# Kernel tuning notes

Hardware: AMD Instinct MI355X
Metric: run time of the kernel (lower is better)

Reference implementation:

```python
import jax, jax.numpy as jnp
import numpy as np

B = 256          # graph pairs
S = 128          # max_set_size (all graphs full-size)
D = 64           # node_state_dim (= filters_3)
DE = 32          # encoded edge dim
DM = 128         # message dim
DT = 32          # transform_dim
IN_N, IN_E = 16, 8
EPG = 1024       # edges per graph
NPROP = 5
SINK_ITERS = 20
TEMP = 0.1
N = 2 * B * S    # total nodes
E = 2 * B * EPG  # total edges


def setup_inputs() -> dict:
    key = jax.random.key(0)
    ks = jax.random.split(key, 32)
    def w(k, shp):
        return (jax.random.normal(k, shp, jnp.float32) / np.sqrt(shp[0])).astype(jnp.float32)
    base = jnp.repeat(jnp.arange(2 * B, dtype=jnp.int64) * S, EPG)
    from_idx = base + jax.random.randint(ks[0], (E,), 0, S).astype(jnp.int64)
    to_idx = base + jax.random.randint(ks[1], (E,), 0, S).astype(jnp.int64)
    return {
        'node_features': jax.random.normal(ks[2], (N, IN_N), jnp.float32),
        'edge_features': jax.random.normal(ks[3], (E, IN_E), jnp.float32),
        'W_enc_n': w(ks[4], (IN_N, D)),  'b_enc_n': jnp.zeros((D,), jnp.float32),
        'W_enc_e': w(ks[5], (IN_E, DE)), 'b_enc_e': jnp.zeros((DE,), jnp.float32),
        'W_c1': w(ks[6], (2 * D, 2 * D)), 'b_c1': jnp.zeros((2 * D,), jnp.float32),
        'W_c2': w(ks[7], (2 * D, D)),     'b_c2': jnp.zeros((D,), jnp.float32),
        'W_m1': w(ks[8], (2 * D + DE, DM)), 'b_m1': jnp.zeros((DM,), jnp.float32),
        'W_m2': w(ks[9], (DM, DM)),         'b_m2': jnp.zeros((DM,), jnp.float32),
        'W_u1': w(ks[10], (D + DM, DM)), 'b_u1': jnp.zeros((DM,), jnp.float32),
        'W_u2': w(ks[11], (DM, D)),      'b_u2': jnp.zeros((D,), jnp.float32),
        'W_t1': w(ks[12], (D, DT)), 'b_t1': jnp.zeros((DT,), jnp.float32),
        'W_t2': w(ks[13], (DT, DT)), 'b_t2': jnp.zeros((DT,), jnp.float32),
        'from_idx': from_idx, 'to_idx': to_idx,
    }


def _sinkhorn(sim):
    # log-space sinkhorn normalization, fixed iteration count
    log_a = sim / TEMP
    for _ in range(SINK_ITERS):
        log_a = log_a - jax.nn.logsumexp(log_a, axis=2, keepdims=True)
        log_a = log_a - jax.nn.logsumexp(log_a, axis=1, keepdims=True)
    return jnp.exp(log_a)


def reference(node_features, edge_features, W_enc_n, b_enc_n, W_enc_e, b_enc_e,
              W_c1, b_c1, W_c2, b_c2, W_m1, b_m1, W_m2, b_m2,
              W_u1, b_u1, W_u2, b_u2, W_t1, b_t1, W_t2, b_t2,
              from_idx, to_idx):
    h_enc = node_features @ W_enc_n + b_enc_n          # [N, D]
    e_enc = edge_features @ W_enc_e + b_enc_e          # [E, DE]

    def prop(h):
        # bidirectional messages, shared params (GMN GraphPropLayer, mlp update)
        hf, ht = h[from_idx], h[to_idx]
        m_f = jnp.concatenate([hf, ht, e_enc], -1)
        m_f = jax.nn.relu(m_f @ W_m1 + b_m1) @ W_m2 + b_m2
        m_r = jnp.concatenate([ht, hf, e_enc], -1)
        m_r = jax.nn.relu(m_r @ W_m1 + b_m1) @ W_m2 + b_m2
        agg = jax.ops.segment_sum(m_f, to_idx, num_segments=N) \
            + jax.ops.segment_sum(m_r, from_idx, num_segments=N)
        u = jnp.concatenate([h, agg], -1)
        return jax.nn.relu(u @ W_u1 + b_u1) @ W_u2 + b_u2

    h = h_enc
    store = jnp.zeros_like(h_enc)
    for _ in range(NPROP):
        comb = jnp.concatenate([h, store], -1)
        comb = jax.nn.relu(comb @ W_c1 + b_c1) @ W_c2 + b_c2
        h = prop(comb)                                  # [N, D]
        padded = h.reshape(2 * B, S, D)                 # full graphs -> pad is reshape
        q, c = padded[0::2], padded[1::2]               # [B, S, D] each
        tq = jax.nn.relu(q @ W_t1 + b_t1) @ W_t2 + b_t2
        tc = jax.nn.relu(c @ W_t1 + b_t1) @ W_t2 + b_t2
        # masks are all-ones since every graph has S nodes
        sim = jnp.einsum('bid,bjd->bij', tq, tc)        # [B, S, S]
        T = _sinkhorn(sim)
        q_from_c = jnp.einsum('bij,bjd->bid', T, c)
        c_from_q = jnp.einsum('bij,bid->bjd', T, q)
        # interleave q0,c0,q1,c1,... then gather by node_indices (= arange here)
        store = jnp.stack([q_from_c, c_from_q], axis=1).reshape(N, D)
    scores = -jnp.sum(jax.nn.relu(q - jnp.einsum('bij,bjd->bid', T, c)), axis=(1, 2))
    return scores
```

## Files before the change

kernel.cpp:

```cpp
#include <hip/hip_runtime.h>
#include <hip/hip_bf16.h>

#define NNODE  65536
#define NEDGE  524288
#define NGRAPH 512
#define EPG    1024
#define NPROP  5
#define SINKI  20

typedef __attribute__((ext_vector_type(4))) float f32x4;
typedef __attribute__((ext_vector_type(8))) _Float16 f16x8;

template<int IN, int OUT>
__global__ void enc_kernel(const float* __restrict__ x, const float* __restrict__ W,
                           const float* __restrict__ b, float* __restrict__ y, int rows) {
    int idx = blockIdx.x * blockDim.x + threadIdx.x;
    if (idx >= rows * OUT) return;
    int r = idx / OUT, o = idx % OUT;
    const float* xr = x + (size_t)r * IN;
    float acc = b[o];
#pragma unroll
    for (int k = 0; k < IN; ++k) acc = fmaf(xr[k], W[k * OUT + o], acc);
    y[idx] = acc;
}

template<int IN1, int IN2, int HID, int OUT>
__global__ __launch_bounds__(256) void mlp2_kernel(
    const float* __restrict__ x1, const float* __restrict__ x2,
    const float* __restrict__ W1, const float* __restrict__ b1,
    const float* __restrict__ W2, const float* __restrict__ b2,
    float* __restrict__ y) {
    constexpr int IN = IN1 + IN2;
    constexpr int TR = 64;
    __shared__ float xs[TR][IN];
    __shared__ float hs[TR][HID];
    const int t = threadIdx.x;
    const int row0 = blockIdx.x * TR;

    constexpr int INQ = IN / 4;
    for (int idx = t; idx < TR * INQ; idx += 256) {
        int r = idx / INQ, k0 = (idx % INQ) * 4;
        float4 v;
        if (IN2 == 0 || k0 < IN1) v = *(const float4*)(x1 + (size_t)(row0 + r) * IN1 + k0);
        else                      v = *(const float4*)(x2 + (size_t)(row0 + r) * IN2 + (k0 - IN1));
        *(float4*)&xs[r][k0] = v;
    }
    __syncthreads();

    constexpr int HQ = HID / 4;
    for (int idx = t; idx < TR * HQ; idx += 256) {
        int r = idx / HQ, j0 = (idx % HQ) * 4;
        float a0 = b1[j0], a1 = b1[j0+1], a2 = b1[j0+2], a3 = b1[j0+3];
        const float* wp = W1 + j0;
#pragma unroll 8
        for (int k = 0; k < IN; ++k) {
            float xv = xs[r][k];
            float4 w = *(const float4*)(wp + k * HID);
            a0 = fmaf(xv, w.x, a0); a1 = fmaf(xv, w.y, a1);
            a2 = fmaf(xv, w.z, a2); a3 = fmaf(xv, w.w, a3);
        }
        hs[r][j0]   = fmaxf(a0, 0.f); hs[r][j0+1] = fmaxf(a1, 0.f);
        hs[r][j0+2] = fmaxf(a2, 0.f); hs[r][j0+3] = fmaxf(a3, 0.f);
    }
    __syncthreads();

    constexpr int OQ = OUT / 4;
    for (int idx = t; idx < TR * OQ; idx += 256) {
        int r = idx / OQ, d0 = (idx % OQ) * 4;
        float a0 = b2[d0], a1 = b2[d0+1], a2 = b2[d0+2], a3 = b2[d0+3];
        const float* wp = W2 + d0;
#pragma unroll 8
        for (int k = 0; k < HID; ++k) {
            float hv = hs[r][k];
            float4 w = *(const float4*)(wp + k * OUT);
            a0 = fmaf(hv, w.x, a0); a1 = fmaf(hv, w.y, a1);
            a2 = fmaf(hv, w.z, a2); a3 = fmaf(hv, w.w, a3);
        }
        *(float4*)(y + (size_t)(row0 + r) * OUT + d0) = make_float4(a0, a1, a2, a3);
    }
}

union __align__(16) MsgSMem {
    struct {
        float ag[128][128];
        _Float16 csh[128 * 64];
        _Float16 csl[128 * 64];
        _Float16 Hh[64 * 128];
        _Float16 Hl[64 * 128];
        int ef[1024];
        int et[1024];
    } run;
    _Float16 w1p[2][128 * 160];
    _Float16 w2p[2][128 * 128];
};

__global__ __launch_bounds__(512, 2) void msg_kernel(
    const float* __restrict__ c, const float* __restrict__ e_enc,
    const int* __restrict__ from_idx, const int* __restrict__ to_idx,
    const float* __restrict__ W1, const float* __restrict__ b1,
    const float* __restrict__ W2, const float* __restrict__ b2,
    float* __restrict__ agg) {
    __shared__ MsgSMem sm;
    const int g = blockIdx.x, t = threadIdx.x;
    const int l = t & 63, wid = t >> 6;
    const int rg = wid >> 2;
    const int cg = wid & 3;
    const int lr = l & 15;
    const int lk = (l >> 4) * 8;
    const int ebase = g * EPG, nbase = g * 128;

    for (int idx = t; idx < 160 * 128; idx += 512) {
        int k = idx >> 7, cc = idx & 127;
        float v = W1[idx];
        _Float16 h = (_Float16)v;
        sm.w1p[0][cc * 160 + k] = h;
        sm.w1p[1][cc * 160 + k] = (_Float16)(v - (float)h);
    }
    __syncthreads();
    f16x8 b1h[5][2], b1l[5][2];
#pragma unroll
    for (int kf = 0; kf < 5; ++kf)
#pragma unroll
        for (int cf = 0; cf < 2; ++cf) {
            const int col = cg * 32 + cf * 16 + lr;
            b1h[kf][cf] = *(const f16x8*)&sm.w1p[0][col * 160 + kf * 32 + lk];
            b1l[kf][cf] = *(const f16x8*)&sm.w1p[1][col * 160 + kf * 32 + lk];
        }
    const float b1v0 = b1[cg * 32 + lr], b1v1 = b1[cg * 32 + 16 + lr];
    __syncthreads();

    for (int idx = t; idx < 128 * 128; idx += 512) {
        int k = idx >> 7, cc = idx & 127;
        float v = W2[idx];
        _Float16 h = (_Float16)v;
        sm.w2p[0][cc * 128 + k] = h;
        sm.w2p[1][cc * 128 + k] = (_Float16)(v - (float)h);
    }
    __syncthreads();
    f16x8 b2h[4][2], b2l[4][2];
#pragma unroll
    for (int kf = 0; kf < 4; ++kf)
#pragma unroll
        for (int cf = 0; cf < 2; ++cf) {
            const int col = cg * 32 + cf * 16 + lr;
            b2h[kf][cf] = *(const f16x8*)&sm.w2p[0][col * 128 + kf * 32 + lk];
            b2l[kf][cf] = *(const f16x8*)&sm.w2p[1][col * 128 + kf * 32 + lk];
        }
    const float b2v0 = b2[cg * 32 + lr], b2v1 = b2[cg * 32 + 16 + lr];
    __syncthreads();

    for (int idx = t; idx < 4096; idx += 512)
        ((float4*)sm.run.ag)[idx] = make_float4(0.f, 0.f, 0.f, 0.f);
    {
        const float* cblk = c + (size_t)nbase * 64;
        char* cshB = (char*)sm.run.csh;
        char* cslB = (char*)sm.run.csl;
        for (int idx = t; idx < 128 * 64; idx += 512) {
            int row = idx >> 6, cc = idx & 63;
            float v = cblk[idx];
            _Float16 h = (_Float16)v;
            int byte = ((row << 7) | (cc << 1)) ^ ((row & 7) << 4);
            *(_Float16*)(cshB + byte) = h;
            *(_Float16*)(cslB + byte) = (_Float16)(v - (float)h);
        }
    }
    for (int idx = t; idx < 1024; idx += 512) {
        sm.run.ef[idx] = from_idx[ebase + idx] - nbase;
        sm.run.et[idx] = to_idx[ebase + idx] - nbase;
    }
    __syncthreads();

    char* cshB = (char*)sm.run.csh;
    char* cslB = (char*)sm.run.csl;
    char* HhB  = (char*)sm.run.Hh;
    char* HlB  = (char*)sm.run.Hl;

    for (int tile = 0; tile < 32; ++tile) {
        f32x4 acc[2][2];
#pragma unroll
        for (int rf = 0; rf < 2; ++rf) {
            const int rloc = rg * 32 + rf * 16 + lr;
            const int R = tile * 64 + rloc;
            const int el = R >> 1, dir = R & 1;
            const int fi = sm.run.ef[el], ti = sm.run.et[el];
            const int rA = dir ? ti : fi;
            const int rB = dir ? fi : ti;
            const int swA = (rA & 7) << 4, swB = (rB & 7) << 4;
            f16x8 ah[5], al[5];
            ah[0] = *(const f16x8*)(cshB + (((rA << 7) | (lk << 1)) ^ swA));
            al[0] = *(const f16x8*)(cslB + (((rA << 7) | (lk << 1)) ^ swA));
            ah[1] = *(const f16x8*)(cshB + (((rA << 7) | ((32 + lk) << 1)) ^ swA));
            al[1] = *(const f16x8*)(cslB + (((rA << 7) | ((32 + lk) << 1)) ^ swA));
            ah[2] = *(const f16x8*)(cshB + (((rB << 7) | (lk << 1)) ^ swB));
            al[2] = *(const f16x8*)(cslB + (((rB << 7) | (lk << 1)) ^ swB));
            ah[3] = *(const f16x8*)(cshB + (((rB << 7) | ((32 + lk) << 1)) ^ swB));
            al[3] = *(const f16x8*)(cslB + (((rB << 7) | ((32 + lk) << 1)) ^ swB));
            {
                const float* eE = e_enc + (size_t)(ebase + el) * 32 + lk;
                const float4 e0 = *(const float4*)eE;
                const float4 e1 = *(const float4*)(eE + 4);
                float ev[8] = {e0.x, e0.y, e0.z, e0.w, e1.x, e1.y, e1.z, e1.w};
                f16x8 h8, l8;
#pragma unroll
                for (int j = 0; j < 8; ++j) {
                    _Float16 h = (_Float16)ev[j];
                    h8[j] = h;
                    l8[j] = (_Float16)(ev[j] - (float)h);
                }
                ah[4] = h8; al[4] = l8;
            }
            acc[rf][0] = (f32x4){b1v0, b1v0, b1v0, b1v0};
            acc[rf][1] = (f32x4){b1v1, b1v1, b1v1, b1v1};
#pragma unroll
            for (int kf = 0; kf < 5; ++kf)
#pragma unroll
                for (int cf = 0; cf < 2; ++cf) {
                    acc[rf][cf] = __builtin_amdgcn_mfma_f32_16x16x32_f16(ah[kf], b1h[kf][cf], acc[rf][cf], 0, 0, 0);
                    acc[rf][cf] = __builtin_amdgcn_mfma_f32_16x16x32_f16(al[kf], b1h[kf][cf], acc[rf][cf], 0, 0, 0);
                    acc[rf][cf] = __builtin_amdgcn_mfma_f32_16x16x32_f16(ah[kf], b1l[kf][cf], acc[rf][cf], 0, 0, 0);
                }
        }
        __syncthreads();
#pragma unroll
        for (int rf = 0; rf < 2; ++rf)
#pragma unroll
            for (int cf = 0; cf < 2; ++cf) {
                const int col = cg * 32 + cf * 16 + lr;
#pragma unroll
                for (int q = 0; q < 4; ++q) {
                    const int row = rg * 32 + rf * 16 + (l >> 4) * 4 + q;
                    const int byte = ((row << 8) | (col << 1)) ^ ((row & 7) << 4);
                    float v = fmaxf(acc[rf][cf][q], 0.f);
                    _Float16 h = (_Float16)v;
                    *(_Float16*)(HhB + byte) = h;
                    *(_Float16*)(HlB + byte) = (_Float16)(v - (float)h);
                }
            }
        __syncthreads();

#pragma unroll
        for (int rf = 0; rf < 2; ++rf) {
            const int row = rg * 32 + rf * 16 + lr;
            const int sw = (row & 7) << 4;
            f16x8 xh[4], xl[4];
#pragma unroll
            for (int kf = 0; kf < 4; ++kf) {
                const int byte = ((row << 8) | ((kf * 32 + lk) << 1)) ^ sw;
                xh[kf] = *(const f16x8*)(HhB + byte);
                xl[kf] = *(const f16x8*)(HlB + byte);
            }
            f32x4 acc2[2];
            acc2[0] = (f32x4){b2v0, b2v0, b2v0, b2v0};
            acc2[1] = (f32x4){b2v1, b2v1, b2v1, b2v1};
#pragma unroll
            for (int kf = 0; kf < 4; ++kf)
#pragma unroll
                for (int cf = 0; cf < 2; ++cf) {
                    acc2[cf] = __builtin_amdgcn_mfma_f32_16x16x32_f16(xh[kf], b2h[kf][cf], acc2[cf], 0, 0, 0);
                    acc2[cf] = __builtin_amdgcn_mfma_f32_16x16x32_f16(xl[kf], b2h[kf][cf], acc2[cf], 0, 0, 0);
                    acc2[cf] = __builtin_amdgcn_mfma_f32_16x16x32_f16(xh[kf], b2l[kf][cf], acc2[cf], 0, 0, 0);
                }
            const int r0 = rg * 32 + rf * 16 + ((l >> 4) << 2);
            const int e0 = (tile * 64 + r0) >> 1;
            int dst[4];
            dst[0] = sm.run.et[e0];
            dst[1] = sm.run.ef[e0];
            dst[2] = sm.run.et[e0 + 1];
            dst[3] = sm.run.ef[e0 + 1];
#pragma unroll
            for (int q = 0; q < 4; ++q)
#pragma unroll
                for (int cf = 0; cf < 2; ++cf)
                    atomicAdd(&sm.run.ag[dst[q]][cg * 32 + cf * 16 + lr], acc2[cf][q]);
        }
    }
    __syncthreads();
    float* aout = agg + (size_t)g * 128 * 128;
    for (int idx = t; idx < 4096; idx += 512)
        ((float4*)aout)[idx] = ((const float4*)sm.run.ag)[idx];
}

__global__ __launch_bounds__(256) void sink_kernel(
    const float* __restrict__ tbuf, const float* __restrict__ h,
    float* __restrict__ store, float* __restrict__ scores, int do_score) {
    __shared__ float la[128][128];
    __shared__ float ub[2 * 128 * 66];
    __shared__ float pm[256], ps[256];
    const int p = blockIdx.x, t = threadIdx.x;

    const float* tq_src = tbuf + (size_t)(2 * p)     * 128 * 32;
    const float* tc_src = tbuf + (size_t)(2 * p + 1) * 128 * 32;
    for (int idx = t; idx < 4096; idx += 256) {
        int i = idx >> 5, k = idx & 31;
        ub[i * 33 + k]            = tq_src[idx];
        ub[128 * 33 + i * 33 + k] = tc_src[idx];
    }
    __syncthreads();

    for (int idx = t; idx < 16384; idx += 256) {
        int i = idx >> 7, j = idx & 127;
        float acc = 0.f;
#pragma unroll
        for (int k = 0; k < 32; ++k)
            acc = fmaf(ub[i * 33 + k], ub[128 * 33 + j * 33 + k], acc);
        la[i][j] = acc * 10.f;
    }
    __syncthreads();

    const int w = t >> 6, l = t & 63;
    for (int iter = 0; iter < SINKI; ++iter) {
        for (int r = w; r < 128; r += 4) {
            float a0 = la[r][l], a1 = la[r][l + 64];
            float mx = fmaxf(a0, a1);
#pragma unroll
            for (int off = 32; off >= 1; off >>= 1) mx = fmaxf(mx, __shfl_xor(mx, off));
            float s = __expf(a0 - mx) + __expf(a1 - mx);
#pragma unroll
            for (int off = 32; off >= 1; off >>= 1) s += __shfl_xor(s, off);
            float lse = mx + __logf(s);
            la[r][l]      = a0 - lse;
            la[r][l + 64] = a1 - lse;
        }
        __syncthreads();
        const int j = t & 127, hh = t >> 7, i0 = hh * 64;
        float mx = -INFINITY;
        for (int i = i0; i < i0 + 64; ++i) mx = fmaxf(mx, la[i][j]);
        pm[t] = mx;
        __syncthreads();
        const float M = fmaxf(pm[j], pm[128 + j]);
        float s = 0.f;
        for (int i = i0; i < i0 + 64; ++i) s += __expf(la[i][j] - M);
        ps[t] = s;
        __syncthreads();
        const float lse = M + __logf(ps[j] + ps[128 + j]);
        for (int i = i0; i < i0 + 64; ++i) la[i][j] -= lse;
        __syncthreads();
    }

    for (int idx = t; idx < 16384; idx += 256)
        ((float*)la)[idx] = __expf(((float*)la)[idx]);
    const float* hq_src = h + (size_t)(2 * p)     * 128 * 64;
    const float* hc_src = h + (size_t)(2 * p + 1) * 128 * 64;
    for (int idx = t; idx < 8192; idx += 256) {
        int i = idx >> 6, d = idx & 63;
        ub[i * 66 + d]            = hq_src[idx];
        ub[128 * 66 + i * 66 + d] = hc_src[idx];
    }
    __syncthreads();

    float sc = 0.f;
    float* store_q = store + (size_t)(2 * p)     * 128 * 64;
    float* store_c = store + (size_t)(2 * p + 1) * 128 * 64;
    for (int idx = t; idx < 8192; idx += 256) {
        int i = idx >> 6, d = idx & 63;
        float acc = 0.f;
#pragma unroll 8
        for (int j = 0; j < 128; ++j)
            acc = fmaf(la[i][j], ub[128 * 66 + j * 66 + d], acc);
        store_q[idx] = acc;
        if (do_score) sc += fmaxf(ub[i * 66 + d] - acc, 0.f);
    }
    for (int idx = t; idx < 8192; idx += 256) {
        int j = idx >> 6, d = idx & 63;
        float acc = 0.f;
#pragma unroll 8
        for (int i = 0; i < 128; ++i)
            acc = fmaf(la[i][j], ub[i * 66 + d], acc);
        store_c[idx] = acc;
    }
    if (do_score) {
#pragma unroll
        for (int off = 32; off >= 1; off >>= 1) sc += __shfl_xor(sc, off);
        if (l == 0) pm[w] = sc;
        __syncthreads();
        if (t == 0) scores[p] = -(pm[0] + pm[1] + pm[2] + pm[3]);
    }
}

extern "C" void kernel_launch(void* const* d_in, const int* in_sizes, int n_in,
                              void* d_out, int out_size, void* d_ws, size_t ws_size,
                              hipStream_t stream) {
    const float* node_features = (const float*)d_in[0];
    const float* edge_features = (const float*)d_in[1];
    const float* W_enc_n = (const float*)d_in[2];
    const float* b_enc_n = (const float*)d_in[3];
    const float* W_enc_e = (const float*)d_in[4];
    const float* b_enc_e = (const float*)d_in[5];
    const float* W_c1 = (const float*)d_in[6];
    const float* b_c1 = (const float*)d_in[7];
    const float* W_c2 = (const float*)d_in[8];
    const float* b_c2 = (const float*)d_in[9];
    const float* W_m1 = (const float*)d_in[10];
    const float* b_m1 = (const float*)d_in[11];
    const float* W_m2 = (const float*)d_in[12];
    const float* b_m2 = (const float*)d_in[13];
    const float* W_u1 = (const float*)d_in[14];
    const float* b_u1 = (const float*)d_in[15];
    const float* W_u2 = (const float*)d_in[16];
    const float* b_u2 = (const float*)d_in[17];
    const float* W_t1 = (const float*)d_in[18];
    const float* b_t1 = (const float*)d_in[19];
    const float* W_t2 = (const float*)d_in[20];
    const float* b_t2 = (const float*)d_in[21];
    const int* from_idx = (const int*)d_in[22];
    const int* to_idx   = (const int*)d_in[23];
    float* scores = (float*)d_out;

    char* ws = (char*)d_ws;
    size_t off = 0;
    auto alloc = [&](size_t nfloats) { float* pp = (float*)(ws + off); off += nfloats * sizeof(float); return pp; };
    float* h    = alloc((size_t)NNODE * 64);
    float* st   = alloc((size_t)NNODE * 64);
    float* cbuf = alloc((size_t)NNODE * 64);
    float* aggb = alloc((size_t)NNODE * 128);
    float* tb   = alloc((size_t)NNODE * 32);
    float* eenc = alloc((size_t)NEDGE * 32);
    (void)ws_size; (void)in_sizes; (void)n_in; (void)out_size;

    hipMemsetAsync(st, 0, (size_t)NNODE * 64 * sizeof(float), stream);
    enc_kernel<16, 64><<<(NNODE * 64 + 255) / 256, 256, 0, stream>>>(node_features, W_enc_n, b_enc_n, h, NNODE);
    enc_kernel<8, 32><<<(NEDGE * 32 + 255) / 256, 256, 0, stream>>>(edge_features, W_enc_e, b_enc_e, eenc, NEDGE);

    for (int it = 0; it < NPROP; ++it) {
        mlp2_kernel<64, 64, 128, 64><<<NNODE / 64, 256, 0, stream>>>(h, st, W_c1, b_c1, W_c2, b_c2, cbuf);
        msg_kernel<<<NGRAPH, 512, 0, stream>>>(cbuf, eenc, from_idx, to_idx, W_m1, b_m1, W_m2, b_m2, aggb);
        mlp2_kernel<64, 128, 128, 64><<<NNODE / 64, 256, 0, stream>>>(cbuf, aggb, W_u1, b_u1, W_u2, b_u2, h);
        mlp2_kernel<64, 0, 32, 32><<<NNODE / 64, 256, 0, stream>>>(h, nullptr, W_t1, b_t1, W_t2, b_t2, tb);
        sink_kernel<<<256, 256, 0, stream>>>(tb, h, st, scores, it == NPROP - 1 ? 1 : 0);
    }
}
```

Baseline: 9.295 ms.

## Presplit message weights and edge encodings, shrink MLP tiles, widen sinkhorn blocks

The fp16 hi/lo splitting of the message MLP weights and edge encodings moves out of every msg_kernel block into one-time prep kernels. Weights now load straight from global into registers, and the shared-memory union is dropped. Hidden activations are stored packed hi/lo in one array, and the aggregation buffer gets an XOR swizzle against bank conflicts. The MLP row tile halves to 32 to launch more blocks, and sinkhorn uses 512 threads with a 4-way column reduction. Together these add extra launches and more shared-memory pressure per block, which may change occupancy.

Measured after the change: 8.210 ms. 1.13x faster.

```diff
diff --git a/kernel.cpp b/kernel.cpp
--- a/kernel.cpp
+++ b/kernel.cpp
@@ -10,6 +10,32 @@
 
 typedef __attribute__((ext_vector_type(4))) float f32x4;
 typedef __attribute__((ext_vector_type(8))) _Float16 f16x8;
+
+static __device__ __forceinline__ void split2(float v, _Float16& h, _Float16& l) {
+    h = (_Float16)v;
+    l = (_Float16)(v - (float)h);
+}
+
+static __device__ __forceinline__ unsigned packsplit(float v) {
+    _Float16 h = (_Float16)v;
+    _Float16 lo2 = (_Float16)(v - (float)h);
+    union { _Float16 f; unsigned short s; } uh, ul;
+    uh.f = h; ul.f = lo2;
+    return (unsigned)uh.s | ((unsigned)ul.s << 16);
+}
+
+static __device__ __forceinline__ void unpack8(uint4 a, uint4 b, f16x8& h, f16x8& l) {
+    union { unsigned u[4]; f16x8 v; } H, L;
+    H.u[0] = (a.x & 0xffffu) | (a.y << 16);
+    H.u[1] = (a.z & 0xffffu) | (a.w << 16);
+    H.u[2] = (b.x & 0xffffu) | (b.y << 16);
+    H.u[3] = (b.z & 0xffffu) | (b.w << 16);
+    L.u[0] = (a.x >> 16) | (a.y & 0xffff0000u);
+    L.u[1] = (a.z >> 16) | (a.w & 0xffff0000u);
+    L.u[2] = (b.x >> 16) | (b.y & 0xffff0000u);
+    L.u[3] = (b.z >> 16) | (b.w & 0xffff0000u);
+    h = H.v; l = L.v;
+}
 
 template<int IN, int OUT>
 __global__ void enc_kernel(const float* __restrict__ x, const float* __restrict__ W,
@@ -24,6 +50,31 @@
     y[idx] = acc;
 }
 
+template<int IN, int OUT>
+__global__ void enc_split_kernel(const float* __restrict__ x, const float* __restrict__ W,
+                                 const float* __restrict__ b,
+                                 _Float16* __restrict__ yh, _Float16* __restrict__ yl, int rows) {
+    int idx = blockIdx.x * blockDim.x + threadIdx.x;
+    if (idx >= rows * OUT) return;
+    int r = idx / OUT, o = idx % OUT;
+    const float* xr = x + (size_t)r * IN;
+    float acc = b[o];
+#pragma unroll
+    for (int k = 0; k < IN; ++k) acc = fmaf(xr[k], W[k * OUT + o], acc);
+    _Float16 h, l; split2(acc, h, l);
+    yh[idx] = h; yl[idx] = l;
+}
+
+__global__ void splitT_kernel(const float* __restrict__ W, _Float16* __restrict__ Wh,
+                              _Float16* __restrict__ Wl, int K, int C) {
+    int idx = blockIdx.x * blockDim.x + threadIdx.x;
+    if (idx >= K * C) return;
+    int k = idx / C, cc = idx % C;
+    _Float16 h, l; split2(W[idx], h, l);
+    Wh[(size_t)cc * K + k] = h;
+    Wl[(size_t)cc * K + k] = l;
+}
+
 template<int IN1, int IN2, int HID, int OUT>
 __global__ __launch_bounds__(256) void mlp2_kernel(
     const float* __restrict__ x1, const float* __restrict__ x2,
@@ -31,7 +82,7 @@
     const float* __restrict__ W2, const float* __restrict__ b2,
     float* __restrict__ y) {
     constexpr int IN = IN1 + IN2;
-    constexpr int TR = 64;
+    constexpr int TR = 32;
     __shared__ float xs[TR][IN];
     __shared__ float hs[TR][HID];
     const int t = threadIdx.x;
@@ -59,8 +110,8 @@
             a0 = fmaf(xv, w.x, a0); a1 = fmaf(xv, w.y, a1);
             a2 = fmaf(xv, w.z, a2); a3 = fmaf(xv, w.w, a3);
         }
-        hs[r][j0]   = fmaxf(a0, 0.f); hs[r][j0+1] = fmaxf(a1, 0.f);
-        hs[r][j0+2] = fmaxf(a2, 0.f); hs[r][j0+3] = fmaxf(a3, 0.f);
+        *(float4*)&hs[r][j0] = make_float4(fmaxf(a0, 0.f), fmaxf(a1, 0.f),
+                                           fmaxf(a2, 0.f), fmaxf(a3, 0.f));
     }
     __syncthreads();
 
@@ -80,100 +131,64 @@
     }
 }
 
-union __align__(16) MsgSMem {
-    struct {
-        float ag[128][128];
-        _Float16 csh[128 * 64];
-        _Float16 csl[128 * 64];
-        _Float16 Hh[64 * 128];
-        _Float16 Hl[64 * 128];
-        int ef[1024];
-        int et[1024];
-    } run;
-    _Float16 w1p[2][128 * 160];
-    _Float16 w2p[2][128 * 128];
-};
-
 __global__ __launch_bounds__(512, 2) void msg_kernel(
-    const float* __restrict__ c, const float* __restrict__ e_enc,
+    const float* __restrict__ c,
+    const _Float16* __restrict__ eh, const _Float16* __restrict__ el,
     const int* __restrict__ from_idx, const int* __restrict__ to_idx,
-    const float* __restrict__ W1, const float* __restrict__ b1,
-    const float* __restrict__ W2, const float* __restrict__ b2,
+    const _Float16* __restrict__ W1h, const _Float16* __restrict__ W1l, const float* __restrict__ b1,
+    const _Float16* __restrict__ W2h, const _Float16* __restrict__ W2l, const float* __restrict__ b2,
     float* __restrict__ agg) {
-    __shared__ MsgSMem sm;
+    __shared__ float ag[128][128];
+    __shared__ _Float16 csh[128 * 64];
+    __shared__ _Float16 csl[128 * 64];
+    __shared__ unsigned Hp[64 * 128];
+    __shared__ int ef[1024], et[1024];
     const int g = blockIdx.x, t = threadIdx.x;
     const int l = t & 63, wid = t >> 6;
-    const int rg = wid >> 2;
-    const int cg = wid & 3;
-    const int lr = l & 15;
-    const int lk = (l >> 4) * 8;
+    const int rg = wid >> 2, cg = wid & 3;
+    const int lr = l & 15, lk = (l >> 4) * 8;
     const int ebase = g * EPG, nbase = g * 128;
 
-    for (int idx = t; idx < 160 * 128; idx += 512) {
-        int k = idx >> 7, cc = idx & 127;
-        float v = W1[idx];
-        _Float16 h = (_Float16)v;
-        sm.w1p[0][cc * 160 + k] = h;
-        sm.w1p[1][cc * 160 + k] = (_Float16)(v - (float)h);
-    }
-    __syncthreads();
-    f16x8 b1h[5][2], b1l[5][2];
+    f16x8 b1h[5][2], b1l[5][2], b2h[4][2], b2l[4][2];
 #pragma unroll
     for (int kf = 0; kf < 5; ++kf)
 #pragma unroll
         for (int cf = 0; cf < 2; ++cf) {
-            const int col = cg * 32 + cf * 16 + lr;
-            b1h[kf][cf] = *(const f16x8*)&sm.w1p[0][col * 160 + kf * 32 + lk];
-            b1l[kf][cf] = *(const f16x8*)&sm.w1p[1][col * 160 + kf * 32 + lk];
-        }
-    const float b1v0 = b1[cg * 32 + lr], b1v1 = b1[cg * 32 + 16 + lr];
-    __syncthreads();
-
-    for (int idx = t; idx < 128 * 128; idx += 512) {
-        int k = idx >> 7, cc = idx & 127;
-        float v = W2[idx];
-        _Float16 h = (_Float16)v;
-        sm.w2p[0][cc * 128 + k] = h;
-        sm.w2p[1][cc * 128 + k] = (_Float16)(v - (float)h);
-    }
-    __syncthreads();
-    f16x8 b2h[4][2], b2l[4][2];
+            int col = cg * 32 + cf * 16 + lr;
+            b1h[kf][cf] = *(const f16x8*)&W1h[(size_t)col * 160 + kf * 32 + lk];
+            b1l[kf][cf] = *(const f16x8*)&W1l[(size_t)col * 160 + kf * 32 + lk];
+        }
 #pragma unroll
     for (int kf = 0; kf < 4; ++kf)
 #pragma unroll
         for (int cf = 0; cf < 2; ++cf) {
-            const int col = cg * 32 + cf * 16 + lr;
-            b2h[kf][cf] = *(const f16x8*)&sm.w2p[0][col * 128 + kf * 32 + lk];
-            b2l[kf][cf] = *(const f16x8*)&sm.w2p[1][col * 128 + kf * 32 + lk];
-        }
-    const float b2v0 = b2[cg * 32 + lr], b2v1 = b2[cg * 32 + 16 + lr];
-    __syncthreads();
+            int col = cg * 32 + cf * 16 + lr;
+            b2h[kf][cf] = *(const f16x8*)&W2h[(size_t)col * 128 + kf * 32 + lk];
+            b2l[kf][cf] = *(const f16x8*)&W2l[(size_t)col * 128 + kf * 32 + lk];
+        }
+    const float b1v[2] = { b1[cg * 32 + lr], b1[cg * 32 + 16 + lr] };
+    const float b2v[2] = { b2[cg * 32 + lr], b2[cg * 32 + 16 + lr] };
 
     for (int idx = t; idx < 4096; idx += 512)
-        ((float4*)sm.run.ag)[idx] = make_float4(0.f, 0.f, 0.f, 0.f);
+        ((float4*)ag)[idx] = make_float4(0.f, 0.f, 0.f, 0.f);
     {
         const float* cblk = c + (size_t)nbase * 64;
-        char* cshB = (char*)sm.run.csh;
-        char* cslB = (char*)sm.run.csl;
-        for (int idx = t; idx < 128 * 64; idx += 512) {
-            int row = idx >> 6, cc = idx & 63;
-            float v = cblk[idx];
-            _Float16 h = (_Float16)v;
-            int byte = ((row << 7) | (cc << 1)) ^ ((row & 7) << 4);
-            *(_Float16*)(cshB + byte) = h;
-            *(_Float16*)(cslB + byte) = (_Float16)(v - (float)h);
+        char* chB = (char*)csh; char* clB = (char*)csl;
+        for (int idx = t; idx < 8192; idx += 512) {
+            int row = idx >> 6, k = idx & 63;
+            _Float16 h, lo2; split2(cblk[idx], h, lo2);
+            int byte = ((row << 7) | (k << 1)) ^ ((row & 7) << 4);
+            *(_Float16*)(chB + byte) = h;
+            *(_Float16*)(clB + byte) = lo2;
         }
     }
     for (int idx = t; idx < 1024; idx += 512) {
-        sm.run.ef[idx] = from_idx[ebase + idx] - nbase;
-        sm.run.et[idx] = to_idx[ebase + idx] - nbase;
-    }
-    __syncthreads();
-
-    char* cshB = (char*)sm.run.csh;
-    char* cslB = (char*)sm.run.csl;
-    char* HhB  = (char*)sm.run.Hh;
-    char* HlB  = (char*)sm.run.Hl;
+        ef[idx] = from_idx[ebase + idx] - nbase;
+        et[idx] = to_idx[ebase + idx] - nbase;
+    }
+    __syncthreads();
+
+    char* chB = (char*)csh; char* clB = (char*)csl;
 
     for (int tile = 0; tile < 32; ++tile) {
         f32x4 acc[2][2];
@@ -181,36 +196,23 @@
         for (int rf = 0; rf < 2; ++rf) {
             const int rloc = rg * 32 + rf * 16 + lr;
             const int R = tile * 64 + rloc;
-            const int el = R >> 1, dir = R & 1;
-            const int fi = sm.run.ef[el], ti = sm.run.et[el];
-            const int rA = dir ? ti : fi;
-            const int rB = dir ? fi : ti;
+            const int e2 = R >> 1, dir = R & 1;
+            const int fi = ef[e2], ti = et[e2];
+            const int rA = dir ? ti : fi, rB = dir ? fi : ti;
             const int swA = (rA & 7) << 4, swB = (rB & 7) << 4;
             f16x8 ah[5], al[5];
-            ah[0] = *(const f16x8*)(cshB + (((rA << 7) | (lk << 1)) ^ swA));
-            al[0] = *(const f16x8*)(cslB + (((rA << 7) | (lk << 1)) ^ swA));
-            ah[1] = *(const f16x8*)(cshB + (((rA << 7) | ((32 + lk) << 1)) ^ swA));
-            al[1] = *(const f16x8*)(cslB + (((rA << 7) | ((32 + lk) << 1)) ^ swA));
-            ah[2] = *(const f16x8*)(cshB + (((rB << 7) | (lk << 1)) ^ swB));
-            al[2] = *(const f16x8*)(cslB + (((rB << 7) | (lk << 1)) ^ swB));
-            ah[3] = *(const f16x8*)(cshB + (((rB << 7) | ((32 + lk) << 1)) ^ swB));
-            al[3] = *(const f16x8*)(cslB + (((rB << 7) | ((32 + lk) << 1)) ^ swB));
-            {
-                const float* eE = e_enc + (size_t)(ebase + el) * 32 + lk;
-                const float4 e0 = *(const float4*)eE;
-                const float4 e1 = *(const float4*)(eE + 4);
-                float ev[8] = {e0.x, e0.y, e0.z, e0.w, e1.x, e1.y, e1.z, e1.w};
-                f16x8 h8, l8;
-#pragma unroll
-                for (int j = 0; j < 8; ++j) {
-                    _Float16 h = (_Float16)ev[j];
-                    h8[j] = h;
-                    l8[j] = (_Float16)(ev[j] - (float)h);
-                }
-                ah[4] = h8; al[4] = l8;
-            }
-            acc[rf][0] = (f32x4){b1v0, b1v0, b1v0, b1v0};
-            acc[rf][1] = (f32x4){b1v1, b1v1, b1v1, b1v1};
+            ah[0] = *(const f16x8*)(chB + (((rA << 7) | (lk << 1)) ^ swA));
+            al[0] = *(const f16x8*)(clB + (((rA << 7) | (lk << 1)) ^ swA));
+            ah[1] = *(const f16x8*)(chB + (((rA << 7) | ((32 + lk) << 1)) ^ swA));
+            al[1] = *(const f16x8*)(clB + (((rA << 7) | ((32 + lk) << 1)) ^ swA));
+            ah[2] = *(const f16x8*)(chB + (((rB << 7) | (lk << 1)) ^ swB));
+            al[2] = *(const f16x8*)(clB + (((rB << 7) | (lk << 1)) ^ swB));
+            ah[3] = *(const f16x8*)(chB + (((rB << 7) | ((32 + lk) << 1)) ^ swB));
+            al[3] = *(const f16x8*)(clB + (((rB << 7) | ((32 + lk) << 1)) ^ swB));
+            ah[4] = *(const f16x8*)&eh[(size_t)(ebase + e2) * 32 + lk];
+            al[4] = *(const f16x8*)&el[(size_t)(ebase + e2) * 32 + lk];
+            acc[rf][0] = (f32x4){b1v[0], b1v[0], b1v[0], b1v[0]};
+            acc[rf][1] = (f32x4){b1v[1], b1v[1], b1v[1], b1v[1]};
 #pragma unroll
             for (int kf = 0; kf < 5; ++kf)
 #pragma unroll
@@ -229,75 +231,69 @@
 #pragma unroll
                 for (int q = 0; q < 4; ++q) {
                     const int row = rg * 32 + rf * 16 + (l >> 4) * 4 + q;
-                    const int byte = ((row << 8) | (col << 1)) ^ ((row & 7) << 4);
-                    float v = fmaxf(acc[rf][cf][q], 0.f);
-                    _Float16 h = (_Float16)v;
-                    *(_Float16*)(HhB + byte) = h;
-                    *(_Float16*)(HlB + byte) = (_Float16)(v - (float)h);
+                    Hp[(row * 128 + col) ^ ((row & 7) << 2)] = packsplit(fmaxf(acc[rf][cf][q], 0.f));
                 }
             }
         __syncthreads();
-
 #pragma unroll
         for (int rf = 0; rf < 2; ++rf) {
             const int row = rg * 32 + rf * 16 + lr;
-            const int sw = (row & 7) << 4;
-            f16x8 xh[4], xl[4];
+            const int sw = (row & 7) << 2;
+            f32x4 acc2[2];
+            acc2[0] = (f32x4){b2v[0], b2v[0], b2v[0], b2v[0]};
+            acc2[1] = (f32x4){b2v[1], b2v[1], b2v[1], b2v[1]};
 #pragma unroll
             for (int kf = 0; kf < 4; ++kf) {
-                const int byte = ((row << 8) | ((kf * 32 + lk) << 1)) ^ sw;
-                xh[kf] = *(const f16x8*)(HhB + byte);
-                xl[kf] = *(const f16x8*)(HlB + byte);
+                const int c0 = kf * 32 + lk;
+                uint4 pa = *(const uint4*)&Hp[(row * 128 + c0) ^ sw];
+                uint4 pb = *(const uint4*)&Hp[(row * 128 + c0 + 4) ^ sw];
+                f16x8 xh, xl; unpack8(pa, pb, xh, xl);
+#pragma unroll
+                for (int cf = 0; cf < 2; ++cf) {
+                    acc2[cf] = __builtin_amdgcn_mfma_f32_16x16x32_f16(xh, b2h[kf][cf], acc2[cf], 0, 0, 0);
+                    acc2[cf] = __builtin_amdgcn_mfma_f32_16x16x32_f16(xl, b2h[kf][cf], acc2[cf], 0, 0, 0);
+                    acc2[cf] = __builtin_amdgcn_mfma_f32_16x16x32_f16(xh, b2l[kf][cf], acc2[cf], 0, 0, 0);
+                }
             }
-            f32x4 acc2[2];
-            acc2[0] = (f32x4){b2v0, b2v0, b2v0, b2v0};
-            acc2[1] = (f32x4){b2v1, b2v1, b2v1, b2v1};
-#pragma unroll
-            for (int kf = 0; kf < 4; ++kf)
-#pragma unroll
-                for (int cf = 0; cf < 2; ++cf) {
-                    acc2[cf] = __builtin_amdgcn_mfma_f32_16x16x32_f16(xh[kf], b2h[kf][cf], acc2[cf], 0, 0, 0);
-                    acc2[cf] = __builtin_amdgcn_mfma_f32_16x16x32_f16(xl[kf], b2h[kf][cf], acc2[cf], 0, 0, 0);
-                    acc2[cf] = __builtin_amdgcn_mfma_f32_16x16x32_f16(xh[kf], b2l[kf][cf], acc2[cf], 0, 0, 0);
-                }
             const int r0 = rg * 32 + rf * 16 + ((l >> 4) << 2);
             const int e0 = (tile * 64 + r0) >> 1;
-            int dst[4];
-            dst[0] = sm.run.et[e0];
-            dst[1] = sm.run.ef[e0];
-            dst[2] = sm.run.et[e0 + 1];
-            dst[3] = sm.run.ef[e0 + 1];
+            int dst[4] = { et[e0], ef[e0], et[e0 + 1], ef[e0 + 1] };
 #pragma unroll
             for (int q = 0; q < 4; ++q)
 #pragma unroll
-                for (int cf = 0; cf < 2; ++cf)
-                    atomicAdd(&sm.run.ag[dst[q]][cg * 32 + cf * 16 + lr], acc2[cf][q]);
+                for (int cf = 0; cf < 2; ++cf) {
+                    const int colq = cg * 32 + cf * 16 + lr;
+                    atomicAdd(&ag[dst[q]][colq ^ ((dst[q] & 7) << 2)], acc2[cf][q]);
+                }
         }
     }
     __syncthreads();
     float* aout = agg + (size_t)g * 128 * 128;
-    for (int idx = t; idx < 4096; idx += 512)
-        ((float4*)aout)[idx] = ((const float4*)sm.run.ag)[idx];
-}
-
-__global__ __launch_bounds__(256) void sink_kernel(
+    for (int idx = t; idx < 4096; idx += 512) {
+        int row = idx >> 5, c4 = (idx & 31) << 2;
+        ((float4*)aout)[idx] = *(const float4*)&ag[row][c4 ^ ((row & 7) << 2)];
+    }
+}
+
+__global__ __launch_bounds__(512) void sink_kernel(
     const float* __restrict__ tbuf, const float* __restrict__ h,
     float* __restrict__ store, float* __restrict__ scores, int do_score) {
     __shared__ float la[128][128];
     __shared__ float ub[2 * 128 * 66];
-    __shared__ float pm[256], ps[256];
+    __shared__ float pm[512], ps[512];
     const int p = blockIdx.x, t = threadIdx.x;
+    const int w = t >> 6, l = t & 63;
 
     const float* tq_src = tbuf + (size_t)(2 * p)     * 128 * 32;
     const float* tc_src = tbuf + (size_t)(2 * p + 1) * 128 * 32;
-    for (int idx = t; idx < 4096; idx += 256) {
+    for (int idx = t; idx < 4096; idx += 512) {
         int i = idx >> 5, k = idx & 31;
         ub[i * 33 + k]            = tq_src[idx];
         ub[128 * 33 + i * 33 + k] = tc_src[idx];
     }
     __syncthreads();
 
-    for (int idx = t; idx < 16384; idx += 256) {
+    for (int idx = t; idx < 16384; idx += 512) {
         int i = idx >> 7, j = idx & 127;
         float acc = 0.f;
 #pragma unroll
@@ -307,9 +303,8 @@
     }
     __syncthreads();
 
-    const int w = t >> 6, l = t & 63;
     for (int iter = 0; iter < SINKI; ++iter) {
-        for (int r = w; r < 128; r += 4) {
+        for (int r = w; r < 128; r += 8) {
             float a0 = la[r][l], a1 = la[r][l + 64];
             float mx = fmaxf(a0, a1);
 #pragma unroll
@@ -322,26 +317,26 @@
             la[r][l + 64] = a1 - lse;
         }
         __syncthreads();
-        const int j = t & 127, hh = t >> 7, i0 = hh * 64;
+        const int j = t & 127, q4 = t >> 7, i0 = q4 * 32;
         float mx = -INFINITY;
-        for (int i = i0; i < i0 + 64; ++i) mx = fmaxf(mx, la[i][j]);
+        for (int i = i0; i < i0 + 32; ++i) mx = fmaxf(mx, la[i][j]);
         pm[t] = mx;
         __syncthreads();
-        const float M = fmaxf(pm[j], pm[128 + j]);
+        const float M = fmaxf(fmaxf(pm[j], pm[j + 128]), fmaxf(pm[j + 256], pm[j + 384]));
         float s = 0.f;
-        for (int i = i0; i < i0 + 64; ++i) s += __expf(la[i][j] - M);
+        for (int i = i0; i < i0 + 32; ++i) s += __expf(la[i][j] - M);
         ps[t] = s;
         __syncthreads();
-        const float lse = M + __logf(ps[j] + ps[128 + j]);
-        for (int i = i0; i < i0 + 64; ++i) la[i][j] -= lse;
-        __syncthreads();
-    }
-
-    for (int idx = t; idx < 16384; idx += 256)
+        const float lse = M + __logf(ps[j] + ps[j + 128] + ps[j + 256] + ps[j + 384]);
+        for (int i = i0; i < i0 + 32; ++i) la[i][j] -= lse;
+        __syncthreads();
+    }
+
+    for (int idx = t; idx < 16384; idx += 512)
         ((float*)la)[idx] = __expf(((float*)la)[idx]);
     const float* hq_src = h + (size_t)(2 * p)     * 128 * 64;
     const float* hc_src = h + (size_t)(2 * p + 1) * 128 * 64;
-    for (int idx = t; idx < 8192; idx += 256) {
+    for (int idx = t; idx < 8192; idx += 512) {
         int i = idx >> 6, d = idx & 63;
         ub[i * 66 + d]            = hq_src[idx];
         ub[128 * 66 + i * 66 + d] = hc_src[idx];
@@ -351,7 +346,7 @@
     float sc = 0.f;
     float* store_q = store + (size_t)(2 * p)     * 128 * 64;
     float* store_c = store + (size_t)(2 * p + 1) * 128 * 64;
-    for (int idx = t; idx < 8192; idx += 256) {
+    for (int idx = t; idx < 8192; idx += 512) {
         int i = idx >> 6, d = idx & 63;
         float acc = 0.f;
 #pragma unroll 8
@@ -360,7 +355,7 @@
         store_q[idx] = acc;
         if (do_score) sc += fmaxf(ub[i * 66 + d] - acc, 0.f);
     }
-    for (int idx = t; idx < 8192; idx += 256) {
+    for (int idx = t; idx < 8192; idx += 512) {
         int j = idx >> 6, d = idx & 63;
         float acc = 0.f;
 #pragma unroll 8
@@ -373,7 +368,12 @@
         for (int off = 32; off >= 1; off >>= 1) sc += __shfl_xor(sc, off);
         if (l == 0) pm[w] = sc;
         __syncthreads();
-        if (t == 0) scores[p] = -(pm[0] + pm[1] + pm[2] + pm[3]);
+        if (t == 0) {
+            float s8 = 0.f;
+#pragma unroll
+            for (int i = 0; i < 8; ++i) s8 += pm[i];
+            scores[p] = -s8;
+        }
     }
 }
 
@@ -408,24 +408,32 @@
 
     char* ws = (char*)d_ws;
     size_t off = 0;
-    auto alloc = [&](size_t nfloats) { float* pp = (float*)(ws + off); off += nfloats * sizeof(float); return pp; };
-    float* h    = alloc((size_t)NNODE * 64);
-    float* st   = alloc((size_t)NNODE * 64);
-    float* cbuf = alloc((size_t)NNODE * 64);
-    float* aggb = alloc((size_t)NNODE * 128);
-    float* tb   = alloc((size_t)NNODE * 32);
-    float* eenc = alloc((size_t)NEDGE * 32);
+    auto alloc = [&](size_t bytes) { char* p = ws + off; off += (bytes + 255) & ~(size_t)255; return p; };
+    float* h    = (float*)alloc((size_t)NNODE * 64 * 4);
+    float* st   = (float*)alloc((size_t)NNODE * 64 * 4);
+    float* cbuf = (float*)alloc((size_t)NNODE * 64 * 4);
+    float* aggb = (float*)alloc((size_t)NNODE * 128 * 4);
+    float* tb   = (float*)alloc((size_t)NNODE * 32 * 4);
+    _Float16* eench = (_Float16*)alloc((size_t)NEDGE * 32 * 2);
+    _Float16* eencl = (_Float16*)alloc((size_t)NEDGE * 32 * 2);
+    _Float16* Wm1h = (_Float16*)alloc(160 * 128 * 2);
+    _Float16* Wm1l = (_Float16*)alloc(160 * 128 * 2);
+    _Float16* Wm2h = (_Float16*)alloc(128 * 128 * 2);
+    _Float16* Wm2l = (_Float16*)alloc(128 * 128 * 2);
     (void)ws_size; (void)in_sizes; (void)n_in; (void)out_size;
 
     hipMemsetAsync(st, 0, (size_t)NNODE * 64 * sizeof(float), stream);
     enc_kernel<16, 64><<<(NNODE * 64 + 255) / 256, 256, 0, stream>>>(node_features, W_enc_n, b_enc_n, h, NNODE);
-    enc_kernel<8, 32><<<(NEDGE * 32 + 255) / 256, 256, 0, stream>>>(edge_features, W_enc_e, b_enc_e, eenc, NEDGE);
+    enc_split_kernel<8, 32><<<(NEDGE * 32 + 255) / 256, 256, 0, stream>>>(edge_features, W_enc_e, b_enc_e, eench, eencl, NEDGE);
+    splitT_kernel<<<(160 * 128 + 255) / 256, 256, 0, stream>>>(W_m1, Wm1h, Wm1l, 160, 128);
+    splitT_kernel<<<(128 * 128 + 255) / 256, 256, 0, stream>>>(W_m2, Wm2h, Wm2l, 128, 128);
 
     for (int it = 0; it < NPROP; ++it) {
-        mlp2_kernel<64, 64, 128, 64><<<NNODE / 64, 256, 0, stream>>>(h, st, W_c1, b_c1, W_c2, b_c2, cbuf);
-        msg_kernel<<<NGRAPH, 512, 0, stream>>>(cbuf, eenc, from_idx, to_idx, W_m1, b_m1, W_m2, b_m2, aggb);
-        mlp2_kernel<64, 128, 128, 64><<<NNODE / 64, 256, 0, stream>>>(cbuf, aggb, W_u1, b_u1, W_u2, b_u2, h);
-        mlp2_kernel<64, 0, 32, 32><<<NNODE / 64, 256, 0, stream>>>(h, nullptr, W_t1, b_t1, W_t2, b_t2, tb);
-        sink_kernel<<<256, 256, 0, stream>>>(tb, h, st, scores, it == NPROP - 1 ? 1 : 0);
-    }
-}
+        mlp2_kernel<64, 64, 128, 64><<<NNODE / 32, 256, 0, stream>>>(h, st, W_c1, b_c1, W_c2, b_c2, cbuf);
+        msg_kernel<<<NGRAPH, 512, 0, stream>>>(
+            cbuf, eench, eencl, from_idx, to_idx, Wm1h, Wm1l, b_m1, Wm2h, Wm2l, b_m2, aggb);
+        mlp2_kernel<64, 128, 128, 64><<<NNODE / 32, 256, 0, stream>>>(cbuf, aggb, W_u1, b_u1, W_u2, b_u2, h);
+        mlp2_kernel<64, 0, 32, 32><<<NNODE / 32, 256, 0, stream>>>(h, nullptr, W_t1, b_t1, W_t2, b_t2, tb);
+        sink_kernel<<<256, 512, 0, stream>>>(tb, h, st, scores, it == NPROP - 1 ? 1 : 0);
+    }
+}
```
